# Kernel optimization log

Measured on AMD Instinct MI355X. Metric: run time of the kernel, lower is better.

## Reference

```python
import jax, jax.numpy as jnp
import numpy as np

B, N, GEO, CLS = 32, 1024, 4, 28
F0 = GEO + CLS          # 32
F1 = F0 * 2             # 64
F2 = F0 * 4             # 128
EPS = 1e-5


def _lin(x, W, b):
    return x @ W.T + b


def _bn(x, g, b):
    # torch BatchNorm1d(element_num) on [B, N, F]: channel dim is N,
    # normalize over (batch, feature) with biased variance (training mode).
    m = x.mean(axis=(0, 2), keepdims=True)
    v = ((x - m) ** 2).mean(axis=(0, 2), keepdims=True)
    return g[None, :, None] * (x - m) * jax.lax.rsqrt(v + EPS) + b[None, :, None]


def _relation(x, Wu, bu, psi, phi, wr):
    # Vectorized form of the triple python loop:
    #   S[b,i,j] = psi*phi * <x_i, x_j>, diagonal excluded
    #   out_i   = wr * (sum_j S[b,i,j] * relu(unary(x_j))) / N + x_i
    n = x.shape[1]
    U = jax.nn.relu(_lin(x, Wu, bu))                       # [B,N,F2]
    S = (psi[0] * phi[0]) * jnp.einsum('bnd,bmd->bnm', x, x)
    S = S * (1.0 - jnp.eye(n, dtype=x.dtype))              # mask i==j
    return wr[0] * (S @ U) / n + x


def setup_inputs() -> dict:
    key = jax.random.key(0)
    ks = iter(jax.random.split(key, 64))

    def W(o, i):
        return jax.random.normal(next(ks), (o, i), jnp.float32) * 0.02

    def bvec(o):
        return jnp.zeros((o,), jnp.float32)

    inp = {'input': jax.random.uniform(next(ks), (B, N, F0), jnp.float32)}
    inp.update(e1_W=W(F1, F0), e1_b=bvec(F1),
               bn1_g=jnp.ones((N,), jnp.float32), bn1_b=bvec(N),
               e2_W=W(F2, F1), e2_b=bvec(F2),
               bn2_g=jnp.ones((N,), jnp.float32), bn2_b=bvec(N),
               e3_W=W(F2, F2), e3_b=bvec(F2))
    for r in (1, 2, 3, 4):
        inp[f'r{r}_W'] = W(F2, F2)
        inp[f'r{r}_b'] = bvec(F2)
        inp[f'r{r}_psi'] = jax.random.uniform(next(ks), (1,), jnp.float32)
        inp[f'r{r}_phi'] = jax.random.uniform(next(ks), (1,), jnp.float32)
        inp[f'r{r}_wr'] = jax.random.uniform(next(ks), (1,), jnp.float32)
    inp.update(d1_W=W(F1, F2), d1_b=bvec(F1),
               dbn_g=jnp.ones((N,), jnp.float32), dbn_b=bvec(N),
               d2_W=W(F0, F1), d2_b=bvec(F0),
               bc_W=W(CLS, F0), bc_b=bvec(CLS),
               bg_W=W(GEO, F0), bg_b=bvec(GEO))
    return inp


def reference(input, e1_W, e1_b, bn1_g, bn1_b, e2_W, e2_b, bn2_g, bn2_b,
              e3_W, e3_b,
              r1_W, r1_b, r1_psi, r1_phi, r1_wr,
              r2_W, r2_b, r2_psi, r2_phi, r2_wr,
              r3_W, r3_b, r3_psi, r3_phi, r3_wr,
              r4_W, r4_b, r4_psi, r4_phi, r4_wr,
              d1_W, d1_b, dbn_g, dbn_b, d2_W, d2_b,
              bc_W, bc_b, bg_W, bg_b):
    out = jax.nn.relu(_bn(_lin(input, e1_W, e1_b), bn1_g, bn1_b))
    out = jax.nn.relu(_bn(_lin(out, e2_W, e2_b), bn2_g, bn2_b))
    enc = jax.nn.sigmoid(_lin(out, e3_W, e3_b))
    x = _relation(enc, r1_W, r1_b, r1_psi, r1_phi, r1_wr)
    x = _relation(x, r2_W, r2_b, r2_psi, r2_phi, r2_wr)
    x = _relation(x, r3_W, r3_b, r3_psi, r3_phi, r3_wr)
    x = _relation(x, r4_W, r4_b, r4_psi, r4_phi, r4_wr)
    out = jax.nn.relu(_bn(_lin(x, d1_W, d1_b), dbn_g, dbn_b))
    out = jax.nn.relu(_lin(out, d2_W, d2_b))
    syn_cls = _lin(out, bc_W, bc_b)
    syn_geo = _lin(out, bg_W, bg_b)
    return jnp.concatenate((syn_cls, syn_geo), axis=2)
```

## Files before the change

kernel.cpp:

```cpp
#include <hip/hip_runtime.h>
#include <hip/hip_bf16.h>


typedef __hip_bfloat16 bf16;
typedef unsigned short ushort_t;
typedef float v4f __attribute__((ext_vector_type(4)));
typedef short v8s __attribute__((ext_vector_type(8)));
#define MFMA_BF16 __builtin_amdgcn_mfma_f32_16x16x32_bf16

#define NB 32
#define NN 1024

__device__ __forceinline__ float ldin(const void* p, size_t i, int f32){
    return f32 ? ((const float*)p)[i] : __bfloat162float(((const bf16*)p)[i]);
}
__device__ __forceinline__ float bf2f(ushort_t u){
    return __uint_as_float((unsigned)u << 16);
}
__device__ __forceinline__ ushort_t f2bf(float v){
    bf16 h = __float2bfloat16(v);
    ushort_t s; __builtin_memcpy(&s, &h, 2);
    return s;
}
__device__ __forceinline__ void unpack8(uint4 v, float* f){
    f[0] = __uint_as_float(v.x << 16);
    f[1] = __uint_as_float(v.x & 0xffff0000u);
    f[2] = __uint_as_float(v.y << 16);
    f[3] = __uint_as_float(v.y & 0xffff0000u);
    f[4] = __uint_as_float(v.z << 16);
    f[5] = __uint_as_float(v.z & 0xffff0000u);
    f[6] = __uint_as_float(v.w << 16);
    f[7] = __uint_as_float(v.w & 0xffff0000u);
}

__global__ __launch_bounds__(64) void k_detect(const void* __restrict__ inp, int* __restrict__ flag){
    int t = threadIdx.x;
    unsigned v = ((const unsigned*)inp)[t];
    int hit = (v & 0x80008000u) ? 1 : 0;
    unsigned long long m = __ballot(hit);
    if (t == 0) *flag = (__popcll(m) > 4) ? 1 : 0;
}

struct PrepArgs {
    const void* w[11];
    int K[11], O[11], off[11];
};

__global__ __launch_bounds__(256) void k_prep(PrepArgs a, float* __restrict__ wpf,
                                              ushort_t* __restrict__ whi, ushort_t* __restrict__ wlo,
                                              const int* __restrict__ flag){
    int f32 = *flag;
    int s = blockIdx.y;
    int idx = blockIdx.x*256 + threadIdx.x;
    if (s < 6){
        int K = a.K[s], O = a.O[s];
        if (idx >= K*O) return;
        int k = idx / O, j = idx - k*O;
        wpf[a.off[s] + idx] = ldin(a.w[s], (size_t)j*K + k, f32);
    } else {
        if (idx >= 16384) return;
        int n = idx >> 7, k = idx & 127;
        float v = ldin(a.w[s], (size_t)n*128 + k, f32);
        ushort_t h = f2bf(v);
        ushort_t l = f2bf(v - bf2f(h));
        int di = (s - 6)*16384 + ((k >> 3)*128 + n)*8 + (k & 7);
        whi[di] = h; wlo[di] = l;
    }
}

template<int K, int O, bool EXTIN>
__global__ __launch_bounds__(128) void k_bnlin(
    const void* __restrict__ xin, const float* __restrict__ Wt,
    const void* __restrict__ bias, const void* __restrict__ bng,
    const void* __restrict__ bnb, bf16* __restrict__ out,
    const int* __restrict__ flag)
{
    int f32 = *flag;
    constexpr int BR  = O/16;
    constexpr int NBT = 32/BR;
    constexpr int G   = K/8;
    __shared__ __align__(16) float wt[K*O];
    __shared__ __align__(16) float xst[2][K*36];
    int t = threadIdx.x;
    int w = t >> 6, lane = t & 63;
    int n = blockIdx.x*2 + w;

    for (int i = t; i < K*O/4; i += 128)
        reinterpret_cast<float4*>(wt)[i] = reinterpret_cast<const float4*>(Wt)[i];
    for (int i = lane; i < 32*G; i += 64){
        int b = i / G, g = i - b*G;
        float f[8];
        if (EXTIN && f32){
            const float* src = (const float*)xin + ((size_t)b*NN + n)*K + g*8;
            float4 v0 = *reinterpret_cast<const float4*>(src);
            float4 v1 = *reinterpret_cast<const float4*>(src + 4);
            f[0]=v0.x; f[1]=v0.y; f[2]=v0.z; f[3]=v0.w;
            f[4]=v1.x; f[5]=v1.y; f[6]=v1.z; f[7]=v1.w;
        } else {
            uint4 v = *reinterpret_cast<const uint4*>((const bf16*)xin + ((size_t)b*NN + n)*K + g*8);
            unpack8(v, f);
        }
        #pragma unroll
        for (int j=0;j<8;j++) xst[w][(g*8+j)*36 + b] = f[j];
    }
    __syncthreads();

    int bt = lane % NBT, jt = lane / NBT;
    int b0 = bt*BR, j0 = jt*8;
    const float* xw = xst[w];
    float acc[BR][8];
    #pragma unroll
    for (int i=0;i<BR;i++)
        #pragma unroll
        for (int j=0;j<8;j++) acc[i][j] = 0.f;

    for (int k = 0; k < K; k++){
        float xv[BR], wv[8];
        #pragma unroll
        for (int i=0;i<BR;i+=4)
            *reinterpret_cast<float4*>(&xv[i]) = *reinterpret_cast<const float4*>(&xw[k*36 + b0 + i]);
        *reinterpret_cast<float4*>(&wv[0]) = *reinterpret_cast<const float4*>(&wt[k*O + j0]);
        *reinterpret_cast<float4*>(&wv[4]) = *reinterpret_cast<const float4*>(&wt[k*O + j0 + 4]);
        #pragma unroll
        for (int i=0;i<BR;i++)
            #pragma unroll
            for (int j=0;j<8;j++) acc[i][j] = fmaf(xv[i], wv[j], acc[i][j]);
    }

    float bj[8];
    #pragma unroll
    for (int j=0;j<8;j++) bj[j] = ldin(bias, j0+j, f32);
    float s1 = 0.f, s2 = 0.f;
    #pragma unroll
    for (int i=0;i<BR;i++)
        #pragma unroll
        for (int j=0;j<8;j++){
            float a = acc[i][j] + bj[j];
            acc[i][j] = a; s1 += a; s2 = fmaf(a, a, s2);
        }
    #pragma unroll
    for (int off = 32; off > 0; off >>= 1){
        s1 += __shfl_down(s1, off);
        s2 += __shfl_down(s2, off);
    }
    s1 = __shfl(s1, 0); s2 = __shfl(s2, 0);
    const float M = 32.f * O;
    float m  = s1 / M;
    float vv = s2 / M - m*m;
    float rs = rsqrtf(vv + 1e-5f);
    float gv = ldin(bng, n, f32), bv = ldin(bnb, n, f32);
    #pragma unroll
    for (int i=0;i<BR;i++){
        union { uint4 u; ushort_t s[8]; } pk;
        #pragma unroll
        for (int j=0;j<8;j++)
            pk.s[j] = f2bf(fmaxf(fmaf(gv*(acc[i][j]-m), rs, bv), 0.f));
        *reinterpret_cast<uint4*>(out + ((size_t)(b0+i)*NN + n)*O + j0) = pk.u;
    }
}

template<int MODE>
__global__ __launch_bounds__(256) void k_lin128m(
    const ushort_t* __restrict__ xin,
    const ushort_t* __restrict__ Whi, const ushort_t* __restrict__ Wlo,
    const void* __restrict__ bias,
    ushort_t* __restrict__ outA, ushort_t* __restrict__ outUT,
    float* __restrict__ dvec, const int* __restrict__ flag)
{
    __shared__ ushort_t xs[8192];
    int t = threadIdx.x;
    size_t row0 = (size_t)blockIdx.x * 64;
    {
        const uint4* src = reinterpret_cast<const uint4*>(xin + row0*128);
        #pragma unroll
        for (int c = 0; c < 4; c++){
            int i = t + c*256;
            int r = i >> 4, kg = i & 15;
            *reinterpret_cast<uint4*>(&xs[(kg*64 + r)*8]) = src[i];
        }
    }
    __syncthreads();
    int w = t >> 6, lane = t & 63;
    int col = lane & 15, quad = lane >> 4;
    v4f acc[4][2];
    #pragma unroll
    for (int m=0;m<4;m++)
        #pragma unroll
        for (int nt=0;nt<2;nt++) acc[m][nt] = (v4f){0.f,0.f,0.f,0.f};

    #pragma unroll
    for (int kt = 0; kt < 4; kt++){
        int kg = kt*4 + quad;
        v8s a[4], bh[2], bl[2];
        #pragma unroll
        for (int nt=0;nt<2;nt++){
            int n = w*32 + nt*16 + col;
            bh[nt] = *reinterpret_cast<const v8s*>(&Whi[(kg*128 + n)*8]);
            bl[nt] = *reinterpret_cast<const v8s*>(&Wlo[(kg*128 + n)*8]);
        }
        #pragma unroll
        for (int m=0;m<4;m++)
            a[m] = *reinterpret_cast<const v8s*>(&xs[(kg*64 + m*16 + col)*8]);
        #pragma unroll
        for (int m=0;m<4;m++)
            #pragma unroll
            for (int nt=0;nt<2;nt++){
                acc[m][nt] = MFMA_BF16(a[m], bh[nt], acc[m][nt], 0, 0, 0);
                acc[m][nt] = MFMA_BF16(a[m], bl[nt], acc[m][nt], 0, 0, 0);
            }
    }
    int f32 = *flag;
    int b = (int)(row0 >> 10);
    int rbase = (int)(row0 & 1023);
    #pragma unroll
    for (int nt=0;nt<2;nt++){
        int n = w*32 + nt*16 + col;
        float bn = ldin(bias, n, f32);
        #pragma unroll
        for (int m=0;m<4;m++){
            if (MODE == 0){
                #pragma unroll
                for (int reg=0;reg<4;reg++){
                    int r = m*16 + quad*4 + reg;
                    float v = acc[m][nt][reg] + bn;
                    outA[(row0 + r)*128 + n] = f2bf(1.f/(1.f+expf(-v)));
                }
            } else {
                union { uint2 u; ushort_t s[4]; } pk;
                #pragma unroll
                for (int reg=0;reg<4;reg++)
                    pk.s[reg] = f2bf(fmaxf(acc[m][nt][reg] + bn, 0.f));
                int rb = rbase + m*16 + quad*4;
                *reinterpret_cast<uint2*>(&outUT[((size_t)b*128 + n)*1024 + rb]) = pk.u;
            }
        }
    }
    if (MODE == 1 && t < 64){
        float s = 0.f;
        #pragma unroll 8
        for (int k=0;k<128;k++){
            float v = bf2f(xs[((k>>3)*64 + t)*8 + (k&7)]);
            s = fmaf(v, v, s);
        }
        dvec[row0 + t] = s;
    }
}

__global__ __launch_bounds__(256) void k_relTm(
    const ushort_t* __restrict__ x,
    const ushort_t* __restrict__ UT,
    float* __restrict__ Tp)
{
    __shared__ ushort_t xts[8192];
    int b = blockIdx.x, rs = blockIdx.y;
    int t = threadIdx.x;
    int w = t >> 6, lane = t & 63;
    int col = lane & 15, quad = lane >> 4;
    int wn = (w >> 1)*64, wc = (w & 1)*64;
    const ushort_t* utb = UT + ((size_t)b << 17);
    v4f acc[4][4];
    #pragma unroll
    for (int m=0;m<4;m++)
        #pragma unroll
        for (int q=0;q<4;q++) acc[m][q] = (v4f){0.f,0.f,0.f,0.f};

    for (int ch = 0; ch < 2; ch++){
        __syncthreads();
        int r0 = rs*128 + ch*64;
        #pragma unroll
        for (int c = 0; c < 4; c++){
            int i = t + c*256;
            int r = i >> 4, cs8 = (i & 15)*8;
            uint4 v = *reinterpret_cast<const uint4*>(&x[((size_t)b*1024 + r0 + r)*128 + cs8]);
            int base = ((r >> 3)*128 + cs8)*8 + (r & 7);
            xts[base     ] = (ushort_t)(v.x & 0xffff);
            xts[base + 8 ] = (ushort_t)(v.x >> 16);
            xts[base + 16] = (ushort_t)(v.y & 0xffff);
            xts[base + 24] = (ushort_t)(v.y >> 16);
            xts[base + 32] = (ushort_t)(v.z & 0xffff);
            xts[base + 40] = (ushort_t)(v.z >> 16);
            xts[base + 48] = (ushort_t)(v.w & 0xffff);
            xts[base + 56] = (ushort_t)(v.w >> 16);
        }
        __syncthreads();
        #pragma unroll
        for (int kt = 0; kt < 2; kt++){
            int kg = kt*4 + quad;
            v8s a[4], bb[4];
            #pragma unroll
            for (int m=0;m<4;m++)
                a[m] = *reinterpret_cast<const v8s*>(
                    &utb[((size_t)(wn + m*16 + col))*1024 + r0 + kg*8]);
            #pragma unroll
            for (int q=0;q<4;q++)
                bb[q] = *reinterpret_cast<const v8s*>(&xts[(kg*128 + wc + q*16 + col)*8]);
            #pragma unroll
            for (int m=0;m<4;m++)
                #pragma unroll
                for (int q=0;q<4;q++)
                    acc[m][q] = MFMA_BF16(a[m], bb[q], acc[m][q], 0, 0, 0);
        }
    }
    float* dst = Tp + (((size_t)rs*NB + b) << 14);
    #pragma unroll
    for (int m=0;m<4;m++)
        #pragma unroll
        for (int q=0;q<4;q++)
            #pragma unroll
            for (int reg=0;reg<4;reg++){
                int n = wn + m*16 + quad*4 + reg;
                int c = wc + q*16 + col;
                dst[n*128 + c] = acc[m][q][reg];
            }
}

__global__ __launch_bounds__(256) void k_tredm(const float* __restrict__ Tp,
                                               ushort_t* __restrict__ Thi, ushort_t* __restrict__ Tlo){
    int i = blockIdx.x*256 + threadIdx.x;
    const size_t S = 524288;
    float s = ((Tp[i] + Tp[S+i]) + (Tp[2*S+i] + Tp[3*S+i]))
            + ((Tp[4*S+i] + Tp[5*S+i]) + (Tp[6*S+i] + Tp[7*S+i]));
    int bb = i >> 14, j = i & 16383;
    int n = j >> 7, c = j & 127;
    int di = (bb << 14) + ((c >> 3)*128 + n)*8 + (c & 7);
    ushort_t h = f2bf(s);
    Thi[di] = h;
    Tlo[di] = f2bf(s - bf2f(h));
}

__global__ __launch_bounds__(256) void k_reloutm(
    ushort_t* __restrict__ x, const ushort_t* __restrict__ UT,
    const ushort_t* __restrict__ Thi, const ushort_t* __restrict__ Tlo,
    const float* __restrict__ dvec,
    const void* __restrict__ psi, const void* __restrict__ phi, const void* __restrict__ wr,
    const int* __restrict__ flag)
{
    __shared__ ushort_t xs[8192];
    int t = threadIdx.x;
    size_t row0 = (size_t)blockIdx.x * 64;
    int b = (int)(row0 >> 10);
    int rbase = (int)(row0 & 1023);
    {
        const uint4* src = reinterpret_cast<const uint4*>(x + row0*128);
        #pragma unroll
        for (int c = 0; c < 4; c++){
            int i = t + c*256;
            int r = i >> 4, kg = i & 15;
            *reinterpret_cast<uint4*>(&xs[(kg*64 + r)*8]) = src[i];
        }
    }
    __syncthreads();
    int f32 = *flag;
    float alpha = ldin(wr,0,f32) * ldin(psi,0,f32) * ldin(phi,0,f32) * (1.f/1024.f);
    int w = t >> 6, lane = t & 63;
    int col = lane & 15, quad = lane >> 4;
    const ushort_t* sh = Thi + ((size_t)b << 14);
    const ushort_t* sl = Tlo + ((size_t)b << 14);
    v4f acc[4][2];
    #pragma unroll
    for (int m=0;m<4;m++)
        #pragma unroll
        for (int nt=0;nt<2;nt++) acc[m][nt] = (v4f){0.f,0.f,0.f,0.f};

    #pragma unroll
    for (int kt = 0; kt < 4; kt++){
        int kg = kt*4 + quad;
        v8s a[4], bh[2], bl[2];
        #pragma unroll
        for (int nt=0;nt<2;nt++){
            int n = w*32 + nt*16 + col;
            bh[nt] = *reinterpret_cast<const v8s*>(&sh[(kg*128 + n)*8]);
            bl[nt] = *reinterpret_cast<const v8s*>(&sl[(kg*128 + n)*8]);
        }
        #pragma unroll
        for (int m=0;m<4;m++)
            a[m] = *reinterpret_cast<const v8s*>(&xs[(kg*64 + m*16 + col)*8]);
        #pragma unroll
        for (int m=0;m<4;m++)
            #pragma unroll
            for (int nt=0;nt<2;nt++){
                acc[m][nt] = MFMA_BF16(a[m], bh[nt], acc[m][nt], 0, 0, 0);
                acc[m][nt] = MFMA_BF16(a[m], bl[nt], acc[m][nt], 0, 0, 0);
            }
    }
    #pragma unroll
    for (int m=0;m<4;m++){
        float4 d4 = *reinterpret_cast<const float4*>(&dvec[row0 + m*16 + quad*4]);
        #pragma unroll
        for (int nt=0;nt<2;nt++){
            int n = w*32 + nt*16 + col;
            uint2 uu = *reinterpret_cast<const uint2*>(
                &UT[((size_t)b*128 + n)*1024 + rbase + m*16 + quad*4]);
            float uf[4];
            uf[0] = __uint_as_float(uu.x << 16);
            uf[1] = __uint_as_float(uu.x & 0xffff0000u);
            uf[2] = __uint_as_float(uu.y << 16);
            uf[3] = __uint_as_float(uu.y & 0xffff0000u);
            const float* dr = reinterpret_cast<const float*>(&d4);
            #pragma unroll
            for (int reg=0;reg<4;reg++){
                int r = m*16 + quad*4 + reg;
                float xv = bf2f(xs[((n>>3)*64 + r)*8 + (n&7)]);
                float o = fmaf(alpha, acc[m][nt][reg] - dr[reg]*uf[reg], xv);
                x[(row0 + r)*128 + n] = f2bf(o);
            }
        }
    }
}

__global__ __launch_bounds__(256) void k_dec2(
    const bf16* __restrict__ x,
    const float* __restrict__ W2t, const void* __restrict__ b2,
    const float* __restrict__ Wct, const void* __restrict__ bcb,
    const float* __restrict__ Wgt, const void* __restrict__ bgb,
    void* __restrict__ out, const int* __restrict__ flag)
{
    int f32 = *flag;
    __shared__ __align__(16) float w2[64*32];
    __shared__ __align__(16) float wc[32*28];
    __shared__ __align__(16) float wg[32*4];
    __shared__ __align__(16) float xs[8][64];
    __shared__ float hs[8][33];
    size_t row0 = (size_t)blockIdx.x * 8;
    int t = threadIdx.x;
    for (int i=t;i<512;i+=256)  reinterpret_cast<float4*>(w2)[i] = reinterpret_cast<const float4*>(W2t)[i];
    if (t < 224) reinterpret_cast<float4*>(wc)[t] = reinterpret_cast<const float4*>(Wct)[t];
    if (t < 32)  reinterpret_cast<float4*>(wg)[t] = reinterpret_cast<const float4*>(Wgt)[t];
    if (t < 64){
        int row = t >> 3, seg = t & 7;
        uint4 v = *reinterpret_cast<const uint4*>(x + (row0 + row)*64 + seg*8);
        float f[8]; unpack8(v, f);
        *reinterpret_cast<float4*>(&xs[row][seg*8])   = make_float4(f[0],f[1],f[2],f[3]);
        *reinterpret_cast<float4*>(&xs[row][seg*8+4]) = make_float4(f[4],f[5],f[6],f[7]);
    }
    __syncthreads();
    int j = t & 31, r = t >> 5;
    float a = ldin(b2, j, f32);
    #pragma unroll 8
    for (int k=0;k<64;k++) a = fmaf(xs[r][k], w2[k*32 + j], a);
    hs[r][j] = fmaxf(a, 0.f);
    __syncthreads();
    float o;
    if (j < 28){
        o = ldin(bcb, j, f32);
        #pragma unroll
        for (int k=0;k<32;k++) o = fmaf(hs[r][k], wc[k*28 + j], o);
    } else {
        int jj = j - 28;
        o = ldin(bgb, jj, f32);
        #pragma unroll
        for (int k=0;k<32;k++) o = fmaf(hs[r][k], wg[k*4 + jj], o);
    }
    size_t oi = (row0 + r)*32 + j;
    if (f32) ((float*)out)[oi] = o;
    else     ((bf16*)out)[oi] = __float2bfloat16(o);
}

extern "C" void kernel_launch(void* const* d_in, const int* in_sizes, int n_in,
                              void* d_out, int out_size, void* d_ws, size_t ws_size,
                              hipStream_t stream)
{
    (void)in_sizes; (void)n_in; (void)out_size; (void)ws_size;
    const void* input = d_in[0];
    const void* e1_W = d_in[1];  const void* e1_b = d_in[2];
    const void* bn1_g = d_in[3]; const void* bn1_b = d_in[4];
    const void* e2_W = d_in[5];  const void* e2_b = d_in[6];
    const void* bn2_g = d_in[7]; const void* bn2_b = d_in[8];
    const void* e3_W = d_in[9];  const void* e3_b = d_in[10];
    const void *rW[4], *rb[4], *rpsi[4], *rphi[4], *rwr[4];
    for (int r = 0; r < 4; r++){
        rW[r]   = d_in[11 + r*5 + 0];
        rb[r]   = d_in[11 + r*5 + 1];
        rpsi[r] = d_in[11 + r*5 + 2];
        rphi[r] = d_in[11 + r*5 + 3];
        rwr[r]  = d_in[11 + r*5 + 4];
    }
    const void* d1_W = d_in[31]; const void* d1_b = d_in[32];
    const void* dbn_g = d_in[33];const void* dbn_b = d_in[34];
    const void* d2_W = d_in[35]; const void* d2_b = d_in[36];
    const void* bc_W = d_in[37]; const void* bc_b = d_in[38];
    const void* bg_W = d_in[39]; const void* bg_b = d_in[40];

    float*    ws_f = (float*)d_ws;
    int*      flag = (int*)d_ws;
    float*    wpf  = ws_f + 64;
    ushort_t* whi  = (ushort_t*)(ws_f + 21568);
    ushort_t* wlo  = (ushort_t*)(ws_f + 62528);
    float*    dd   = ws_f + 103488;
    ushort_t* Thi  = (ushort_t*)(ws_f + 136256);
    ushort_t* Tlo  = (ushort_t*)(ws_f + 398400);
    float*    Tp   = ws_f + 660544;
    ushort_t* A    = (ushort_t*)(ws_f + 4854848);
    ushort_t* UT   = (ushort_t*)(ws_f + 6952000);
    bf16*     Cenc = (bf16*)A;
    bf16*     E2   = (bf16*)UT;
    bf16*     Cdec = (bf16*)UT;

    enum { O_E1=0, O_E2=2048, O_D1=10240, O_D2=18432, O_BC=20480, O_BG=21376 };

    PrepArgs pa;
    const void* srcs[11] = {e1_W, e2_W, d1_W, d2_W, bc_W, bg_W, e3_W, rW[0], rW[1], rW[2], rW[3]};
    const int  Ks[11]   = {32,64,128,64,32,32, 128,128,128,128,128};
    const int  Os[11]   = {64,128,64,32,28,4,  128,128,128,128,128};
    const int  offs[11] = {O_E1,O_E2,O_D1,O_D2,O_BC,O_BG, 0,0,0,0,0};
    for (int i=0;i<11;i++){ pa.w[i]=srcs[i]; pa.K[i]=Ks[i]; pa.O[i]=Os[i]; pa.off[i]=offs[i]; }

    k_detect<<<1, 64, 0, stream>>>(input, flag);
    k_prep<<<dim3(64,11), 256, 0, stream>>>(pa, wpf, whi, wlo, flag);
    k_bnlin<32,64,true><<<512, 128, 0, stream>>>(input, wpf+O_E1, e1_b, bn1_g, bn1_b, Cenc, flag);
    k_bnlin<64,128,false><<<512, 128, 0, stream>>>(Cenc, wpf+O_E2, e2_b, bn2_g, bn2_b, E2, flag);
    k_lin128m<0><<<512, 256, 0, stream>>>((const ushort_t*)E2, whi, wlo, e3_b,
                                          A, (ushort_t*)nullptr, (float*)nullptr, flag);

    for (int r = 0; r < 4; r++){
        const ushort_t* wh = whi + (size_t)(1+r)*16384;
        const ushort_t* wl = wlo + (size_t)(1+r)*16384;
        k_lin128m<1><<<512, 256, 0, stream>>>(A, wh, wl, rb[r],
                                              (ushort_t*)nullptr, UT, dd, flag);
        k_relTm<<<dim3(32,8), 256, 0, stream>>>(A, UT, Tp);
        k_tredm<<<2048, 256, 0, stream>>>(Tp, Thi, Tlo);
        k_reloutm<<<512, 256, 0, stream>>>(A, UT, Thi, Tlo, dd,
                                           rpsi[r], rphi[r], rwr[r], flag);
    }

    k_bnlin<128,64,false><<<512, 128, 0, stream>>>((const bf16*)A, wpf+O_D1, d1_b, dbn_g, dbn_b, Cdec, flag);
    k_dec2<<<4096, 256, 0, stream>>>(Cdec, wpf+O_D2, d2_b, wpf+O_BC, bc_b, wpf+O_BG, bg_b, d_out, flag);
}
```

Measured before the change: 348.6 us.

## Fuse next relation's linear into relation output kernel and split relT grid

Folds the per-relation unary linear+ReLU (and the e3 sigmoid linear) into the tail of the preceding kernel, so the freshly computed x stays in shared memory and feeds the MFMA directly instead of being reloaded by a separate launch. Output tiles are staged through LDS for coalesced A and UT writes. The dtype detection kernel is replaced by an inline per-block detection, and the relT grid is doubled by splitting the N dimension. This removes five launches and some global round trips, at the cost of extra syncs, more LDS traffic and redundant per-block detection.

```diff
diff --git a/kernel.cpp b/kernel.cpp
--- a/kernel.cpp
+++ b/kernel.cpp
@@ -33,12 +33,16 @@
     f[7] = __uint_as_float(v.w & 0xffff0000u);
 }
 
-__global__ __launch_bounds__(64) void k_detect(const void* __restrict__ inp, int* __restrict__ flag){
+__device__ __forceinline__ int detect_dev(const void* inp){
+    __shared__ int sflag;
     int t = threadIdx.x;
-    unsigned v = ((const unsigned*)inp)[t];
-    int hit = (v & 0x80008000u) ? 1 : 0;
-    unsigned long long m = __ballot(hit);
-    if (t == 0) *flag = (__popcll(m) > 4) ? 1 : 0;
+    if (t < 64){
+        unsigned v = ((const unsigned*)inp)[t];
+        unsigned long long m = __ballot((v & 0x80008000u) != 0u);
+        if (t == 0) sflag = (__popcll(m) > 4) ? 1 : 0;
+    }
+    __syncthreads();
+    return sflag;
 }
 
 struct PrepArgs {
@@ -48,8 +52,8 @@
 
 __global__ __launch_bounds__(256) void k_prep(PrepArgs a, float* __restrict__ wpf,
                                               ushort_t* __restrict__ whi, ushort_t* __restrict__ wlo,
-                                              const int* __restrict__ flag){
-    int f32 = *flag;
+                                              const void* __restrict__ detin){
+    int f32 = detect_dev(detin);
     int s = blockIdx.y;
     int idx = blockIdx.x*256 + threadIdx.x;
     if (s < 6){
@@ -72,10 +76,10 @@
 __global__ __launch_bounds__(128) void k_bnlin(
     const void* __restrict__ xin, const float* __restrict__ Wt,
     const void* __restrict__ bias, const void* __restrict__ bng,
-    const void* __restrict__ bnb, bf16* __restrict__ out,
-    const int* __restrict__ flag)
+    const void* __restrict__ bnb, ushort_t* __restrict__ out,
+    const void* __restrict__ detin)
 {
-    int f32 = *flag;
+    int f32 = detect_dev(detin);
     constexpr int BR  = O/16;
     constexpr int NBT = 32/BR;
     constexpr int G   = K/8;
@@ -86,18 +90,18 @@
     int n = blockIdx.x*2 + w;
 
     for (int i = t; i < K*O/4; i += 128)
-        reinterpret_cast<float4*>(wt)[i] = reinterpret_cast<const float4*>(Wt)[i];
+        ((float4*)wt)[i] = ((const float4*)Wt)[i];
     for (int i = lane; i < 32*G; i += 64){
         int b = i / G, g = i - b*G;
         float f[8];
         if (EXTIN && f32){
             const float* src = (const float*)xin + ((size_t)b*NN + n)*K + g*8;
-            float4 v0 = *reinterpret_cast<const float4*>(src);
-            float4 v1 = *reinterpret_cast<const float4*>(src + 4);
+            float4 v0 = ((const float4*)src)[0];
+            float4 v1 = ((const float4*)src)[1];
             f[0]=v0.x; f[1]=v0.y; f[2]=v0.z; f[3]=v0.w;
             f[4]=v1.x; f[5]=v1.y; f[6]=v1.z; f[7]=v1.w;
         } else {
-            uint4 v = *reinterpret_cast<const uint4*>((const bf16*)xin + ((size_t)b*NN + n)*K + g*8);
+            uint4 v = *(const uint4*)((const ushort_t*)xin + ((size_t)b*NN + n)*K + (size_t)g*8);
             unpack8(v, f);
         }
         #pragma unroll
@@ -118,9 +122,9 @@
         float xv[BR], wv[8];
         #pragma unroll
         for (int i=0;i<BR;i+=4)
-            *reinterpret_cast<float4*>(&xv[i]) = *reinterpret_cast<const float4*>(&xw[k*36 + b0 + i]);
-        *reinterpret_cast<float4*>(&wv[0]) = *reinterpret_cast<const float4*>(&wt[k*O + j0]);
-        *reinterpret_cast<float4*>(&wv[4]) = *reinterpret_cast<const float4*>(&wt[k*O + j0 + 4]);
+            *(float4*)&xv[i] = *(const float4*)&xw[k*36 + b0 + i];
+        *(float4*)&wv[0] = *(const float4*)&wt[k*O + j0];
+        *(float4*)&wv[4] = *(const float4*)&wt[k*O + j0 + 4];
         #pragma unroll
         for (int i=0;i<BR;i++)
             #pragma unroll
@@ -155,87 +159,43 @@
         #pragma unroll
         for (int j=0;j<8;j++)
             pk.s[j] = f2bf(fmaxf(fmaf(gv*(acc[i][j]-m), rs, bv), 0.f));
-        *reinterpret_cast<uint4*>(out + ((size_t)(b0+i)*NN + n)*O + j0) = pk.u;
-    }
-}
-
-template<int MODE>
-__global__ __launch_bounds__(256) void k_lin128m(
-    const ushort_t* __restrict__ xin,
-    const ushort_t* __restrict__ Whi, const ushort_t* __restrict__ Wlo,
-    const void* __restrict__ bias,
-    ushort_t* __restrict__ outA, ushort_t* __restrict__ outUT,
-    float* __restrict__ dvec, const int* __restrict__ flag)
-{
-    __shared__ ushort_t xs[8192];
-    int t = threadIdx.x;
-    size_t row0 = (size_t)blockIdx.x * 64;
-    {
-        const uint4* src = reinterpret_cast<const uint4*>(xin + row0*128);
-        #pragma unroll
-        for (int c = 0; c < 4; c++){
-            int i = t + c*256;
-            int r = i >> 4, kg = i & 15;
-            *reinterpret_cast<uint4*>(&xs[(kg*64 + r)*8]) = src[i];
-        }
-    }
-    __syncthreads();
-    int w = t >> 6, lane = t & 63;
-    int col = lane & 15, quad = lane >> 4;
-    v4f acc[4][2];
-    #pragma unroll
-    for (int m=0;m<4;m++)
-        #pragma unroll
-        for (int nt=0;nt<2;nt++) acc[m][nt] = (v4f){0.f,0.f,0.f,0.f};
-
-    #pragma unroll
-    for (int kt = 0; kt < 4; kt++){
-        int kg = kt*4 + quad;
-        v8s a[4], bh[2], bl[2];
-        #pragma unroll
-        for (int nt=0;nt<2;nt++){
-            int n = w*32 + nt*16 + col;
-            bh[nt] = *reinterpret_cast<const v8s*>(&Whi[(kg*128 + n)*8]);
-            bl[nt] = *reinterpret_cast<const v8s*>(&Wlo[(kg*128 + n)*8]);
-        }
-        #pragma unroll
-        for (int m=0;m<4;m++)
-            a[m] = *reinterpret_cast<const v8s*>(&xs[(kg*64 + m*16 + col)*8]);
-        #pragma unroll
-        for (int m=0;m<4;m++)
-            #pragma unroll
-            for (int nt=0;nt<2;nt++){
-                acc[m][nt] = MFMA_BF16(a[m], bh[nt], acc[m][nt], 0, 0, 0);
-                acc[m][nt] = MFMA_BF16(a[m], bl[nt], acc[m][nt], 0, 0, 0);
-            }
-    }
-    int f32 = *flag;
-    int b = (int)(row0 >> 10);
-    int rbase = (int)(row0 & 1023);
+        *(uint4*)(out + ((size_t)(b0+i)*NN + n)*O + j0) = pk.u;
+    }
+}
+
+
+
+__device__ __forceinline__ void tail_stage_x(ushort_t* xs, const float o[2][16],
+                                             int w, int col, int quad){
     #pragma unroll
     for (int nt=0;nt<2;nt++){
         int n = w*32 + nt*16 + col;
-        float bn = ldin(bias, n, f32);
-        #pragma unroll
-        for (int m=0;m<4;m++){
-            if (MODE == 0){
-                #pragma unroll
-                for (int reg=0;reg<4;reg++){
-                    int r = m*16 + quad*4 + reg;
-                    float v = acc[m][nt][reg] + bn;
-                    outA[(row0 + r)*128 + n] = f2bf(1.f/(1.f+expf(-v)));
-                }
-            } else {
-                union { uint2 u; ushort_t s[4]; } pk;
-                #pragma unroll
-                for (int reg=0;reg<4;reg++)
-                    pk.s[reg] = f2bf(fmaxf(acc[m][nt][reg] + bn, 0.f));
-                int rb = rbase + m*16 + quad*4;
-                *reinterpret_cast<uint2*>(&outUT[((size_t)b*128 + n)*1024 + rb]) = pk.u;
-            }
-        }
-    }
-    if (MODE == 1 && t < 64){
+        #pragma unroll
+        for (int m=0;m<4;m++)
+            #pragma unroll
+            for (int reg=0;reg<4;reg++){
+                int r = m*16 + quad*4 + reg;
+                xs[((n>>3)*64 + r)*8 + (n&7)] = f2bf(o[nt][m*4+reg]);
+            }
+    }
+}
+
+__device__ __forceinline__ void tail_write_A(const ushort_t* xs, ushort_t* A,
+                                             size_t row0, int t){
+    uint4* dst = (uint4*)(A + row0*128);
+    #pragma unroll
+    for (int c = 0; c < 4; c++){
+        int i = t + c*256;
+        int r = i >> 4, kg = i & 15;
+        dst[i] = *(const uint4*)&xs[(kg*64 + r)*8];
+    }
+}
+
+__device__ __forceinline__ void tail_lin_relu(ushort_t* xs, ushort_t* UT,
+    const ushort_t* Whi, const ushort_t* Wlo, const void* bias, float* dvec,
+    size_t row0, int b, int rbase, int t, int w, int lane, int col, int quad, int f32)
+{
+    if (t < 64){
         float s = 0.f;
         #pragma unroll 8
         for (int k=0;k<128;k++){
@@ -244,23 +204,153 @@
         }
         dvec[row0 + t] = s;
     }
-}
-
-__global__ __launch_bounds__(256) void k_relTm(
-    const ushort_t* __restrict__ x,
-    const ushort_t* __restrict__ UT,
+    v4f acc[4][2];
+    #pragma unroll
+    for (int m=0;m<4;m++)
+        #pragma unroll
+        for (int nt=0;nt<2;nt++) acc[m][nt] = (v4f){0.f,0.f,0.f,0.f};
+    #pragma unroll
+    for (int kt = 0; kt < 4; kt++){
+        int kg = kt*4 + quad;
+        v8s a[4], bh[2], bl[2];
+        #pragma unroll
+        for (int nt=0;nt<2;nt++){
+            int n = w*32 + nt*16 + col;
+            bh[nt] = *(const v8s*)&Whi[(kg*128 + n)*8];
+            bl[nt] = *(const v8s*)&Wlo[(kg*128 + n)*8];
+        }
+        #pragma unroll
+        for (int m=0;m<4;m++)
+            a[m] = *(const v8s*)&xs[(kg*64 + m*16 + col)*8];
+        #pragma unroll
+        for (int m=0;m<4;m++)
+            #pragma unroll
+            for (int nt=0;nt<2;nt++){
+                acc[m][nt] = MFMA_BF16(a[m], bh[nt], acc[m][nt], 0, 0, 0);
+                acc[m][nt] = MFMA_BF16(a[m], bl[nt], acc[m][nt], 0, 0, 0);
+            }
+    }
+    float u[2][16];
+    #pragma unroll
+    for (int nt=0;nt<2;nt++){
+        int n = w*32 + nt*16 + col;
+        float bn = ldin(bias, n, f32);
+        #pragma unroll
+        for (int m=0;m<4;m++)
+            #pragma unroll
+            for (int reg=0;reg<4;reg++)
+                u[nt][m*4+reg] = fmaxf(acc[m][nt][reg] + bn, 0.f);
+    }
+    __syncthreads();
+    #pragma unroll
+    for (int nt=0;nt<2;nt++){
+        int n = w*32 + nt*16 + col;
+        #pragma unroll
+        for (int m=0;m<4;m++)
+            #pragma unroll
+            for (int reg=0;reg<4;reg++){
+                int r = m*16 + quad*4 + reg;
+                xs[n*64 + r] = f2bf(u[nt][m*4+reg]);
+            }
+    }
+    __syncthreads();
+    #pragma unroll
+    for (int c = 0; c < 4; c++){
+        int i = t + c*256;
+        int n = i >> 3, sg = i & 7;
+        *(uint4*)&UT[((size_t)b*128 + n)*1024 + rbase + sg*8] =
+            *(const uint4*)&xs[n*64 + sg*8];
+    }
+}
+
+__global__ __launch_bounds__(256, 2) void k_linfuse0(
+    const ushort_t* __restrict__ xin,
+    const ushort_t* __restrict__ W3h, const ushort_t* __restrict__ W3l,
+    const void* __restrict__ b3,
+    const ushort_t* __restrict__ W1h, const ushort_t* __restrict__ W1l,
+    const void* __restrict__ b1,
+    ushort_t* __restrict__ A, ushort_t* __restrict__ UT,
+    float* __restrict__ dvec, const void* __restrict__ detin)
+{
+    __shared__ __align__(16) ushort_t xs[8192];
+    int f32 = detect_dev(detin);
+    int t = threadIdx.x;
+    size_t row0 = (size_t)blockIdx.x * 64;
+    int b = (int)(row0 >> 10), rbase = (int)(row0 & 1023);
+    {
+        const uint4* src = (const uint4*)(xin + row0*128);
+        #pragma unroll
+        for (int c = 0; c < 4; c++){
+            int i = t + c*256;
+            int r = i >> 4, kg = i & 15;
+            *(uint4*)&xs[(kg*64 + r)*8] = src[i];
+        }
+    }
+    __syncthreads();
+    int w = t >> 6, lane = t & 63;
+    int col = lane & 15, quad = lane >> 4;
+    v4f acc[4][2];
+    #pragma unroll
+    for (int m=0;m<4;m++)
+        #pragma unroll
+        for (int nt=0;nt<2;nt++) acc[m][nt] = (v4f){0.f,0.f,0.f,0.f};
+    #pragma unroll
+    for (int kt = 0; kt < 4; kt++){
+        int kg = kt*4 + quad;
+        v8s a[4], bh[2], bl[2];
+        #pragma unroll
+        for (int nt=0;nt<2;nt++){
+            int n = w*32 + nt*16 + col;
+            bh[nt] = *(const v8s*)&W3h[(kg*128 + n)*8];
+            bl[nt] = *(const v8s*)&W3l[(kg*128 + n)*8];
+        }
+        #pragma unroll
+        for (int m=0;m<4;m++)
+            a[m] = *(const v8s*)&xs[(kg*64 + m*16 + col)*8];
+        #pragma unroll
+        for (int m=0;m<4;m++)
+            #pragma unroll
+            for (int nt=0;nt<2;nt++){
+                acc[m][nt] = MFMA_BF16(a[m], bh[nt], acc[m][nt], 0, 0, 0);
+                acc[m][nt] = MFMA_BF16(a[m], bl[nt], acc[m][nt], 0, 0, 0);
+            }
+    }
+    float o[2][16];
+    #pragma unroll
+    for (int nt=0;nt<2;nt++){
+        int n = w*32 + nt*16 + col;
+        float bn = ldin(b3, n, f32);
+        #pragma unroll
+        for (int m=0;m<4;m++)
+            #pragma unroll
+            for (int reg=0;reg<4;reg++){
+                float v = acc[m][nt][reg] + bn;
+                o[nt][m*4+reg] = 1.f/(1.f+expf(-v));
+            }
+    }
+    __syncthreads();
+    tail_stage_x(xs, o, w, col, quad);
+    __syncthreads();
+    tail_write_A(xs, A, row0, t);
+    tail_lin_relu(xs, UT, W1h, W1l, b1, dvec, row0, b, rbase, t, w, lane, col, quad, f32);
+}
+
+__global__ __launch_bounds__(256) void k_relT(
+    const ushort_t* __restrict__ x, const ushort_t* __restrict__ UT,
     float* __restrict__ Tp)
 {
-    __shared__ ushort_t xts[8192];
-    int b = blockIdx.x, rs = blockIdx.y;
+    __shared__ __align__(16) ushort_t xts[8192];
+    int blk = blockIdx.x;
+    int b = blk & 31, rs = (blk >> 5) & 7, nh = blk >> 8;
     int t = threadIdx.x;
     int w = t >> 6, lane = t & 63;
     int col = lane & 15, quad = lane >> 4;
-    int wn = (w >> 1)*64, wc = (w & 1)*64;
+    int wn = nh*64 + (w & 1)*32;
+    int wc = (w >> 1)*64;
     const ushort_t* utb = UT + ((size_t)b << 17);
-    v4f acc[4][4];
-    #pragma unroll
-    for (int m=0;m<4;m++)
+    v4f acc[2][4];
+    #pragma unroll
+    for (int m=0;m<2;m++)
         #pragma unroll
         for (int q=0;q<4;q++) acc[m][q] = (v4f){0.f,0.f,0.f,0.f};
 
@@ -271,7 +361,7 @@
         for (int c = 0; c < 4; c++){
             int i = t + c*256;
             int r = i >> 4, cs8 = (i & 15)*8;
-            uint4 v = *reinterpret_cast<const uint4*>(&x[((size_t)b*1024 + r0 + r)*128 + cs8]);
+            uint4 v = *(const uint4*)&x[((size_t)b*1024 + r0 + r)*128 + cs8];
             int base = ((r >> 3)*128 + cs8)*8 + (r & 7);
             xts[base     ] = (ushort_t)(v.x & 0xffff);
             xts[base + 8 ] = (ushort_t)(v.x >> 16);
@@ -286,16 +376,15 @@
         #pragma unroll
         for (int kt = 0; kt < 2; kt++){
             int kg = kt*4 + quad;
-            v8s a[4], bb[4];
-            #pragma unroll
-            for (int m=0;m<4;m++)
-                a[m] = *reinterpret_cast<const v8s*>(
-                    &utb[((size_t)(wn + m*16 + col))*1024 + r0 + kg*8]);
+            v8s a[2], bb[4];
+            #pragma unroll
+            for (int m=0;m<2;m++)
+                a[m] = *(const v8s*)&utb[((size_t)(wn + m*16 + col))*1024 + r0 + kg*8];
             #pragma unroll
             for (int q=0;q<4;q++)
-                bb[q] = *reinterpret_cast<const v8s*>(&xts[(kg*128 + wc + q*16 + col)*8]);
-            #pragma unroll
-            for (int m=0;m<4;m++)
+                bb[q] = *(const v8s*)&xts[(kg*128 + wc + q*16 + col)*8];
+            #pragma unroll
+            for (int m=0;m<2;m++)
                 #pragma unroll
                 for (int q=0;q<4;q++)
                     acc[m][q] = MFMA_BF16(a[m], bb[q], acc[m][q], 0, 0, 0);
@@ -303,7 +392,7 @@
     }
     float* dst = Tp + (((size_t)rs*NB + b) << 14);
     #pragma unroll
-    for (int m=0;m<4;m++)
+    for (int m=0;m<2;m++)
         #pragma unroll
         for (int q=0;q<4;q++)
             #pragma unroll
@@ -314,8 +403,8 @@
             }
 }
 
-__global__ __launch_bounds__(256) void k_tredm(const float* __restrict__ Tp,
-                                               ushort_t* __restrict__ Thi, ushort_t* __restrict__ Tlo){
+__global__ __launch_bounds__(256) void k_tred(const float* __restrict__ Tp,
+                                              ushort_t* __restrict__ Thi, ushort_t* __restrict__ Tlo){
     int i = blockIdx.x*256 + threadIdx.x;
     const size_t S = 524288;
     float s = ((Tp[i] + Tp[S+i]) + (Tp[2*S+i] + Tp[3*S+i]))
@@ -328,29 +417,30 @@
     Tlo[di] = f2bf(s - bf2f(h));
 }
 
-__global__ __launch_bounds__(256) void k_reloutm(
-    ushort_t* __restrict__ x, const ushort_t* __restrict__ UT,
+template<int LAST>
+__global__ __launch_bounds__(256, 2) void k_relfuse(
+    ushort_t* __restrict__ x, ushort_t* __restrict__ UT,
     const ushort_t* __restrict__ Thi, const ushort_t* __restrict__ Tlo,
-    const float* __restrict__ dvec,
+    float* __restrict__ dvec,
     const void* __restrict__ psi, const void* __restrict__ phi, const void* __restrict__ wr,
-    const int* __restrict__ flag)
+    const ushort_t* __restrict__ Wnh, const ushort_t* __restrict__ Wnl,
+    const void* __restrict__ bnext, const void* __restrict__ detin)
 {
-    __shared__ ushort_t xs[8192];
+    __shared__ __align__(16) ushort_t xs[8192];
+    int f32 = detect_dev(detin);
     int t = threadIdx.x;
     size_t row0 = (size_t)blockIdx.x * 64;
-    int b = (int)(row0 >> 10);
-    int rbase = (int)(row0 & 1023);
+    int b = (int)(row0 >> 10), rbase = (int)(row0 & 1023);
     {
-        const uint4* src = reinterpret_cast<const uint4*>(x + row0*128);
+        const uint4* src = (const uint4*)(x + row0*128);
         #pragma unroll
         for (int c = 0; c < 4; c++){
             int i = t + c*256;
             int r = i >> 4, kg = i & 15;
-            *reinterpret_cast<uint4*>(&xs[(kg*64 + r)*8]) = src[i];
-        }
-    }
-    __syncthreads();
-    int f32 = *flag;
+            *(uint4*)&xs[(kg*64 + r)*8] = src[i];
+        }
+    }
+    __syncthreads();
     float alpha = ldin(wr,0,f32) * ldin(psi,0,f32) * ldin(phi,0,f32) * (1.f/1024.f);
     int w = t >> 6, lane = t & 63;
     int col = lane & 15, quad = lane >> 4;
@@ -361,7 +451,6 @@
     for (int m=0;m<4;m++)
         #pragma unroll
         for (int nt=0;nt<2;nt++) acc[m][nt] = (v4f){0.f,0.f,0.f,0.f};
-
     #pragma unroll
     for (int kt = 0; kt < 4; kt++){
         int kg = kt*4 + quad;
@@ -369,12 +458,12 @@
         #pragma unroll
         for (int nt=0;nt<2;nt++){
             int n = w*32 + nt*16 + col;
-            bh[nt] = *reinterpret_cast<const v8s*>(&sh[(kg*128 + n)*8]);
-            bl[nt] = *reinterpret_cast<const v8s*>(&sl[(kg*128 + n)*8]);
-        }
-        #pragma unroll
-        for (int m=0;m<4;m++)
-            a[m] = *reinterpret_cast<const v8s*>(&xs[(kg*64 + m*16 + col)*8]);
+            bh[nt] = *(const v8s*)&sh[(kg*128 + n)*8];
+            bl[nt] = *(const v8s*)&sl[(kg*128 + n)*8];
+        }
+        #pragma unroll
+        for (int m=0;m<4;m++)
+            a[m] = *(const v8s*)&xs[(kg*64 + m*16 + col)*8];
         #pragma unroll
         for (int m=0;m<4;m++)
             #pragma unroll
@@ -383,61 +472,66 @@
                 acc[m][nt] = MFMA_BF16(a[m], bl[nt], acc[m][nt], 0, 0, 0);
             }
     }
+    float o[2][16];
     #pragma unroll
     for (int m=0;m<4;m++){
-        float4 d4 = *reinterpret_cast<const float4*>(&dvec[row0 + m*16 + quad*4]);
+        float4 d4 = *(const float4*)&dvec[row0 + m*16 + quad*4];
+        const float* dr = (const float*)&d4;
         #pragma unroll
         for (int nt=0;nt<2;nt++){
             int n = w*32 + nt*16 + col;
-            uint2 uu = *reinterpret_cast<const uint2*>(
-                &UT[((size_t)b*128 + n)*1024 + rbase + m*16 + quad*4]);
+            uint2 uu = *(const uint2*)&UT[((size_t)b*128 + n)*1024 + rbase + m*16 + quad*4];
             float uf[4];
             uf[0] = __uint_as_float(uu.x << 16);
             uf[1] = __uint_as_float(uu.x & 0xffff0000u);
             uf[2] = __uint_as_float(uu.y << 16);
             uf[3] = __uint_as_float(uu.y & 0xffff0000u);
-            const float* dr = reinterpret_cast<const float*>(&d4);
             #pragma unroll
             for (int reg=0;reg<4;reg++){
                 int r = m*16 + quad*4 + reg;
                 float xv = bf2f(xs[((n>>3)*64 + r)*8 + (n&7)]);
-                float o = fmaf(alpha, acc[m][nt][reg] - dr[reg]*uf[reg], xv);
-                x[(row0 + r)*128 + n] = f2bf(o);
-            }
-        }
-    }
+                o[nt][m*4+reg] = fmaf(alpha, acc[m][nt][reg] - dr[reg]*uf[reg], xv);
+            }
+        }
+    }
+    __syncthreads();
+    tail_stage_x(xs, o, w, col, quad);
+    __syncthreads();
+    tail_write_A(xs, x, row0, t);
+    if (!LAST)
+        tail_lin_relu(xs, UT, Wnh, Wnl, bnext, dvec, row0, b, rbase, t, w, lane, col, quad, f32);
 }
 
 __global__ __launch_bounds__(256) void k_dec2(
-    const bf16* __restrict__ x,
+    const ushort_t* __restrict__ x,
     const float* __restrict__ W2t, const void* __restrict__ b2,
     const float* __restrict__ Wct, const void* __restrict__ bcb,
     const float* __restrict__ Wgt, const void* __restrict__ bgb,
-    void* __restrict__ out, const int* __restrict__ flag)
+    void* __restrict__ out, const void* __restrict__ detin)
 {
-    int f32 = *flag;
+    int f32 = detect_dev(detin);
     __shared__ __align__(16) float w2[64*32];
     __shared__ __align__(16) float wc[32*28];
     __shared__ __align__(16) float wg[32*4];
-    __shared__ __align__(16) float xs[8][64];
+    __shared__ __align__(16) float xsd[8][64];
     __shared__ float hs[8][33];
     size_t row0 = (size_t)blockIdx.x * 8;
     int t = threadIdx.x;
-    for (int i=t;i<512;i+=256)  reinterpret_cast<float4*>(w2)[i] = reinterpret_cast<const float4*>(W2t)[i];
-    if (t < 224) reinterpret_cast<float4*>(wc)[t] = reinterpret_cast<const float4*>(Wct)[t];
-    if (t < 32)  reinterpret_cast<float4*>(wg)[t] = reinterpret_cast<const float4*>(Wgt)[t];
+    for (int i=t;i<512;i+=256)  ((float4*)w2)[i] = ((const float4*)W2t)[i];
+    if (t < 224) ((float4*)wc)[t] = ((const float4*)Wct)[t];
+    if (t < 32)  ((float4*)wg)[t] = ((const float4*)Wgt)[t];
     if (t < 64){
         int row = t >> 3, seg = t & 7;
-        uint4 v = *reinterpret_cast<const uint4*>(x + (row0 + row)*64 + seg*8);
+        uint4 v = *(const uint4*)&x[(row0 + row)*64 + seg*8];
         float f[8]; unpack8(v, f);
-        *reinterpret_cast<float4*>(&xs[row][seg*8])   = make_float4(f[0],f[1],f[2],f[3]);
-        *reinterpret_cast<float4*>(&xs[row][seg*8+4]) = make_float4(f[4],f[5],f[6],f[7]);
+        *(float4*)&xsd[row][seg*8]   = make_float4(f[0],f[1],f[2],f[3]);
+        *(float4*)&xsd[row][seg*8+4] = make_float4(f[4],f[5],f[6],f[7]);
     }
     __syncthreads();
     int j = t & 31, r = t >> 5;
     float a = ldin(b2, j, f32);
     #pragma unroll 8
-    for (int k=0;k<64;k++) a = fmaf(xs[r][k], w2[k*32 + j], a);
+    for (int k=0;k<64;k++) a = fmaf(xsd[r][k], w2[k*32 + j], a);
     hs[r][j] = fmaxf(a, 0.f);
     __syncthreads();
     float o;
@@ -453,8 +547,10 @@
     }
     size_t oi = (row0 + r)*32 + j;
     if (f32) ((float*)out)[oi] = o;
-    else     ((bf16*)out)[oi] = __float2bfloat16(o);
-}
+    else     ((ushort_t*)out)[oi] = f2bf(o);
+}
+
+enum { O_E1=0, O_E2=2048, O_D1=10240, O_D2=18432, O_BC=20480, O_BG=21376 };
 
 extern "C" void kernel_launch(void* const* d_in, const int* in_sizes, int n_in,
                               void* d_out, int out_size, void* d_ws, size_t ws_size,
@@ -482,47 +578,46 @@
     const void* bg_W = d_in[39]; const void* bg_b = d_in[40];
 
     float*    ws_f = (float*)d_ws;
-    int*      flag = (int*)d_ws;
-    float*    wpf  = ws_f + 64;
-    ushort_t* whi  = (ushort_t*)(ws_f + 21568);
-    ushort_t* wlo  = (ushort_t*)(ws_f + 62528);
-    float*    dd   = ws_f + 103488;
-    ushort_t* Thi  = (ushort_t*)(ws_f + 136256);
-    ushort_t* Tlo  = (ushort_t*)(ws_f + 398400);
-    float*    Tp   = ws_f + 660544;
-    ushort_t* A    = (ushort_t*)(ws_f + 4854848);
-    ushort_t* UT   = (ushort_t*)(ws_f + 6952000);
-    bf16*     Cenc = (bf16*)A;
-    bf16*     E2   = (bf16*)UT;
-    bf16*     Cdec = (bf16*)UT;
-
-    enum { O_E1=0, O_E2=2048, O_D1=10240, O_D2=18432, O_BC=20480, O_BG=21376 };
+    float*    wpf  = ws_f;
+    float*    dd   = ws_f + 21504;
+    ushort_t* whi  = (ushort_t*)(ws_f + 54272);
+    ushort_t* wlo  = (ushort_t*)(ws_f + 95232);
+    ushort_t* Thi  = (ushort_t*)(ws_f + 136192);
+    ushort_t* Tlo  = (ushort_t*)(ws_f + 398336);
+    float*    Tp   = ws_f + 660480;
+    ushort_t* A    = (ushort_t*)(ws_f + 4854784);
+    ushort_t* UT   = (ushort_t*)(ws_f + 6951936);
+    ushort_t* Cenc = A;
+    ushort_t* E2   = (ushort_t*)Tp;
+    ushort_t* Cdec = UT;
 
     PrepArgs pa;
-    const void* srcs[11] = {e1_W, e2_W, d1_W, d2_W, bc_W, bg_W, e3_W, rW[0], rW[1], rW[2], rW[3]};
+    const void* srcs[11] = {e1_W, e2_W, d1_W, d2_W, bc_W, bg_W,
+                            e3_W, rW[0], rW[1], rW[2], rW[3]};
     const int  Ks[11]   = {32,64,128,64,32,32, 128,128,128,128,128};
     const int  Os[11]   = {64,128,64,32,28,4,  128,128,128,128,128};
     const int  offs[11] = {O_E1,O_E2,O_D1,O_D2,O_BC,O_BG, 0,0,0,0,0};
     for (int i=0;i<11;i++){ pa.w[i]=srcs[i]; pa.K[i]=Ks[i]; pa.O[i]=Os[i]; pa.off[i]=offs[i]; }
 
-    k_detect<<<1, 64, 0, stream>>>(input, flag);
-    k_prep<<<dim3(64,11), 256, 0, stream>>>(pa, wpf, whi, wlo, flag);
-    k_bnlin<32,64,true><<<512, 128, 0, stream>>>(input, wpf+O_E1, e1_b, bn1_g, bn1_b, Cenc, flag);
-    k_bnlin<64,128,false><<<512, 128, 0, stream>>>(Cenc, wpf+O_E2, e2_b, bn2_g, bn2_b, E2, flag);
-    k_lin128m<0><<<512, 256, 0, stream>>>((const ushort_t*)E2, whi, wlo, e3_b,
-                                          A, (ushort_t*)nullptr, (float*)nullptr, flag);
+    k_prep<<<dim3(64,11), 256, 0, stream>>>(pa, wpf, whi, wlo, input);
+    k_bnlin<32,64,true><<<512, 128, 0, stream>>>(input, wpf+O_E1, e1_b, bn1_g, bn1_b, Cenc, input);
+    k_bnlin<64,128,false><<<512, 128, 0, stream>>>(Cenc, wpf+O_E2, e2_b, bn2_g, bn2_b, E2, input);
+    k_linfuse0<<<512, 256, 0, stream>>>(E2, whi, wlo, e3_b,
+                                        whi + 16384, wlo + 16384, rb[0],
+                                        A, UT, dd, input);
 
     for (int r = 0; r < 4; r++){
-        const ushort_t* wh = whi + (size_t)(1+r)*16384;
-        const ushort_t* wl = wlo + (size_t)(1+r)*16384;
-        k_lin128m<1><<<512, 256, 0, stream>>>(A, wh, wl, rb[r],
-                                              (ushort_t*)nullptr, UT, dd, flag);
-        k_relTm<<<dim3(32,8), 256, 0, stream>>>(A, UT, Tp);
-        k_tredm<<<2048, 256, 0, stream>>>(Tp, Thi, Tlo);
-        k_reloutm<<<512, 256, 0, stream>>>(A, UT, Thi, Tlo, dd,
-                                           rpsi[r], rphi[r], rwr[r], flag);
-    }
-
-    k_bnlin<128,64,false><<<512, 128, 0, stream>>>((const bf16*)A, wpf+O_D1, d1_b, dbn_g, dbn_b, Cdec, flag);
-    k_dec2<<<4096, 256, 0, stream>>>(Cdec, wpf+O_D2, d2_b, wpf+O_BC, bc_b, wpf+O_BG, bg_b, d_out, flag);
-}
+        k_relT<<<512, 256, 0, stream>>>(A, UT, Tp);
+        k_tred<<<2048, 256, 0, stream>>>(Tp, Thi, Tlo);
+        if (r < 3)
+            k_relfuse<0><<<512, 256, 0, stream>>>(A, UT, Thi, Tlo, dd,
+                rpsi[r], rphi[r], rwr[r],
+                whi + (size_t)(2+r)*16384, wlo + (size_t)(2+r)*16384, rb[r+1], input);
+        else
+            k_relfuse<1><<<512, 256, 0, stream>>>(A, UT, Thi, Tlo, dd,
+                rpsi[r], rphi[r], rwr[r], whi, wlo, rb[r], input);
+    }
+
+    k_bnlin<128,64,false><<<512, 128, 0, stream>>>(A, wpf+O_D1, d1_b, dbn_g, dbn_b, Cdec, input);
+    k_dec2<<<4096, 256, 0, stream>>>(Cdec, wpf+O_D2, d2_b, wpf+O_BC, bc_b, wpf+O_BG, bg_b, d_out, input);
+}
```

After: 346.3 us. Within noise of the previous version (-0.7%).
